# Kernel tuning notes

Hardware: AMD Instinct MI355X
Metric: run time of the kernel (lower is better)

Reference implementation:

```python
import jax, jax.numpy as jnp
import numpy as np

LN_EPS = 1e-5

def _layer_norm(x, g, b):
    mu = jnp.mean(x, axis=-1, keepdims=True)
    var = jnp.mean(jnp.square(x - mu), axis=-1, keepdims=True)
    return (x - mu) * jax.lax.rsqrt(var + LN_EPS) * g + b

def setup_inputs() -> dict:
    key = jax.random.key(0)
    ks = jax.random.split(key, 12)
    B, L, E, H, W = 4, 1024, 1024, 16, 128
    s = 0.02
    return {
        "x": jax.random.normal(ks[0], (B, L, E), dtype=jnp.float32),
        "in_proj_w": jax.random.normal(ks[1], (3 * E, E), dtype=jnp.float32) * s,
        "in_proj_b": jnp.zeros((3 * E,), dtype=jnp.float32),
        "out_proj_w": jax.random.normal(ks[2], (E, E), dtype=jnp.float32) * s,
        "out_proj_b": jnp.zeros((E,), dtype=jnp.float32),
        "ln1_g": jnp.ones((E,), dtype=jnp.float32),
        "ln1_b": jnp.zeros((E,), dtype=jnp.float32),
        "w1": jax.random.normal(ks[3], (4 * E, E), dtype=jnp.float32) * s,
        "b1": jnp.zeros((4 * E,), dtype=jnp.float32),
        "w2": jax.random.normal(ks[4], (E, 4 * E), dtype=jnp.float32) * s,
        "b2": jnp.zeros((E,), dtype=jnp.float32),
        "ln2_g": jnp.ones((E,), dtype=jnp.float32),
        "ln2_b": jnp.zeros((E,), dtype=jnp.float32),
        "n_head": 16,
        "window_size": 128,
    }

def reference(x, in_proj_w, in_proj_b, out_proj_w, out_proj_b,
              ln1_g, ln1_b, w1, b1, w2, b2, ln2_g, ln2_b,
              n_head, window_size):
    B, L, E = x.shape
    H = n_head
    D = E // H
    # qkv projection (torch Linear convention: y = x @ W.T + b)
    qkv = jnp.einsum('ble,fe->blf', x, in_proj_w) + in_proj_b  # [B,L,3E]
    q, k, v = jnp.split(qkv, 3, axis=-1)
    q = q.reshape(B, L, H, D).transpose(0, 2, 1, 3)  # [B,H,L,D]
    k = k.reshape(B, L, H, D).transpose(0, 2, 1, 3)
    v = v.reshape(B, L, H, D).transpose(0, 2, 1, 3)
    scores = jnp.einsum('bhld,bhmd->bhlm', q, k) / np.sqrt(D)  # [B,H,L,L]
    # banded window mask: allowed iff |i-j| <= window_size (same as the double loop)
    idx = jnp.arange(L)
    band = jnp.abs(idx[:, None] - idx[None, :]) <= window_size  # [L,L]
    scores = jnp.where(band[None, None], scores, -jnp.inf)
    attn = jax.nn.softmax(scores, axis=-1)  # [B,H,L,L]
    ctx = jnp.einsum('bhlm,bhmd->bhld', attn, v)  # [B,H,L,D]
    ctx = ctx.transpose(0, 2, 1, 3).reshape(B, L, E)
    attn_out = jnp.einsum('ble,fe->blf', ctx, out_proj_w) + out_proj_b
    attn_weights = jnp.mean(attn, axis=1)  # torch MHA averages heads -> [B,L,L]
    # residual + norm1 (dropout is identity in eval)
    h = _layer_norm(x + attn_out, ln1_g, ln1_b)
    # positionwise FFN
    ff = jnp.einsum('ble,fe->blf', h, w1) + b1
    ff = jax.nn.relu(ff)
    ff = jnp.einsum('blf,ef->ble', ff, w2) + b2
    out = _layer_norm(h + ff, ln2_g, ln2_b)
    return (out, attn_weights)
```

## Files before the change

kernel.cpp:

```cpp
#include <hip/hip_runtime.h>

#define BB 4
#define LL 1024
#define EE 1024
#define HH 16
#define DD 64

typedef __attribute__((ext_vector_type(8))) short short8;
typedef __attribute__((ext_vector_type(4))) float floatx4;

#define PSTR ((size_t)4096 * 1024)

__device__ __forceinline__ float bf2f(short s) {
    union { unsigned u; float f; } c;
    c.u = ((unsigned)(unsigned short)s) << 16;
    return c.f;
}
__device__ __forceinline__ short f2bf(float f) {
    union { float f; unsigned u; } c; c.f = f;
    unsigned r = c.u + 0x7fffu + ((c.u >> 16) & 1u);
    return (short)(r >> 16);
}

__device__ __forceinline__ void async_copy16(const void* g, void* l) {
    __builtin_amdgcn_global_load_lds(
        (const __attribute__((address_space(1))) unsigned int*)g,
        (__attribute__((address_space(3))) unsigned int*)l, 16, 0, 0);
}

__global__ __launch_bounds__(256) void cvt5(
    const float* __restrict__ x, const float* __restrict__ wqkv,
    const float* __restrict__ wo, const float* __restrict__ w1,
    const float* __restrict__ w2,
    short* __restrict__ xb, short* __restrict__ wqkvb, short* __restrict__ wob,
    short* __restrict__ w1b, short* __restrict__ w2b)
{
    int bi = blockIdx.x;
    const float* in; short* out; int base;
    if      (bi <  4096) { in = x;    out = xb;    base = 0;     }
    else if (bi <  7168) { in = wqkv; out = wqkvb; base = 4096;  }
    else if (bi <  8192) { in = wo;   out = wob;   base = 7168;  }
    else if (bi < 12288) { in = w1;   out = w1b;   base = 8192;  }
    else                 { in = w2;   out = w2b;   base = 12288; }
    int i = (bi - base) * 256 + threadIdx.x;
    float4 v = ((const float4*)in)[i];
    unsigned long long u =
          (unsigned long long)(unsigned short)f2bf(v.x)
        | ((unsigned long long)(unsigned short)f2bf(v.y) << 16)
        | ((unsigned long long)(unsigned short)f2bf(v.z) << 32)
        | ((unsigned long long)(unsigned short)f2bf(v.w) << 48);
    ((unsigned long long*)out)[i] = u;
}

template<bool RELU, bool WVT, bool SK>
__global__ __launch_bounds__(512, 2) void gemm256(
    const short* __restrict__ A, const short* __restrict__ Bw,
    const float* __restrict__ bias,
    short* __restrict__ Cb, short* __restrict__ VTp,
    int M, int N, int K, int Ksp)
{
    __shared__ short SH[67584];
    const int tid  = threadIdx.x;
    const int w    = tid >> 6, lane = tid & 63;
    const int fr   = lane & 15, quad = lane >> 4;
    const int wm   = w >> 2,  wn   = w & 3;

    const int gx   = gridDim.x;
    const int flat = blockIdx.y * gx + blockIdx.x;
    const int nwg  = gx * gridDim.y;
    const int q8   = nwg >> 3;
    const int swz  = (flat & 7) * q8 + (flat >> 3);
    const int m0   = (swz % gx) * 256;
    const int n0   = (swz / gx) * 256;

    const int kb = SK ? blockIdx.z * Ksp : 0;
    const int NT = (SK ? Ksp : K) >> 6;

    const int srow = w * 16 + (lane >> 3);
    const int gcol = ((lane & 7) ^ ((lane >> 3) & 7)) * 8;

    auto stage = [&](int s, int h) {
        if (s >= NT) return;
        short* dstb = SH + (s & 1) * 32768 + (h >> 1) * 16384 + (h & 1) * 8192 + w * 1024;
        const short* src = (h < 2)
            ? A  + (size_t)(m0 + h * 128 + srow) * K + kb + s * 64 + gcol
            : Bw + (size_t)(n0 + (h - 2) * 128 + srow) * K + kb + s * 64 + gcol;
        async_copy16(src, dstb);
        async_copy16(src + (size_t)8 * K, dstb + 512);
    };

    floatx4 acc[8][4];
#pragma unroll
    for (int i = 0; i < 8; ++i)
#pragma unroll
        for (int j = 0; j < 4; ++j) acc[i][j] = (floatx4){0.f, 0.f, 0.f, 0.f};

    stage(0, 0); stage(0, 1); stage(0, 2); stage(0, 3);
    stage(1, 0);

    const int posk0 = ((quad    ) ^ (fr & 7)) * 8;
    const int posk1 = ((4 + quad) ^ (fr & 7)) * 8;

    for (int t = 0; t < NT; ++t) {
        if (t < NT - 1) asm volatile("s_waitcnt vmcnt(2)" ::: "memory");
        else            asm volatile("s_waitcnt vmcnt(0)" ::: "memory");
        __builtin_amdgcn_sched_barrier(0);
        __builtin_amdgcn_s_barrier();
        __builtin_amdgcn_sched_barrier(0);

        const short* sA = SH + (t & 1) * 32768 + wm * 8192;
        const short* sB = SH + (t & 1) * 32768 + 16384 + wn * 4096;

        short8 aL[4], aH[4], b0[4], b1[4], a2[4], a3[4];

#pragma unroll
        for (int i = 0; i < 4; ++i) aL[i] = *(const short8*)&sA[(i * 16 + fr) * 64 + posk0];
#pragma unroll
        for (int j = 0; j < 4; ++j) b0[j] = *(const short8*)&sB[(j * 16 + fr) * 64 + posk0];
        stage(t + 1, 1);
        __builtin_amdgcn_s_setprio(1);
#pragma unroll
        for (int i = 0; i < 4; ++i)
#pragma unroll
            for (int j = 0; j < 4; ++j)
                acc[i][j] = __builtin_amdgcn_mfma_f32_16x16x32_bf16(aL[i], b0[j], acc[i][j], 0, 0, 0);
        __builtin_amdgcn_s_setprio(0);

#pragma unroll
        for (int i = 0; i < 4; ++i) aH[i] = *(const short8*)&sA[((i + 4) * 16 + fr) * 64 + posk0];
#pragma unroll
        for (int j = 0; j < 4; ++j) b1[j] = *(const short8*)&sB[(j * 16 + fr) * 64 + posk1];
        stage(t + 1, 2);
        __builtin_amdgcn_s_setprio(1);
#pragma unroll
        for (int i = 0; i < 4; ++i)
#pragma unroll
            for (int j = 0; j < 4; ++j)
                acc[i + 4][j] = __builtin_amdgcn_mfma_f32_16x16x32_bf16(aH[i], b0[j], acc[i + 4][j], 0, 0, 0);
        __builtin_amdgcn_s_setprio(0);

#pragma unroll
        for (int i = 0; i < 4; ++i) a2[i] = *(const short8*)&sA[(i * 16 + fr) * 64 + posk1];
#pragma unroll
        for (int i = 0; i < 4; ++i) a3[i] = *(const short8*)&sA[((i + 4) * 16 + fr) * 64 + posk1];
        stage(t + 1, 3);
        __builtin_amdgcn_s_setprio(1);
#pragma unroll
        for (int i = 0; i < 4; ++i)
#pragma unroll
            for (int j = 0; j < 4; ++j)
                acc[i][j] = __builtin_amdgcn_mfma_f32_16x16x32_bf16(a2[i], b1[j], acc[i][j], 0, 0, 0);
        __builtin_amdgcn_s_setprio(0);

        asm volatile("s_waitcnt lgkmcnt(0)" ::: "memory");
        __builtin_amdgcn_sched_barrier(0);
        __builtin_amdgcn_s_barrier();
        __builtin_amdgcn_sched_barrier(0);

        stage(t + 2, 0);
        __builtin_amdgcn_s_setprio(1);
#pragma unroll
        for (int i = 0; i < 4; ++i)
#pragma unroll
            for (int j = 0; j < 4; ++j)
                acc[i + 4][j] = __builtin_amdgcn_mfma_f32_16x16x32_bf16(a3[i], b1[j], acc[i + 4][j], 0, 0, 0);
        __builtin_amdgcn_s_setprio(0);
    }

    __syncthreads();

    const int cc = lane & 15, rb4 = quad * 4;
#pragma unroll
    for (int i = 0; i < 8; ++i) {
        int row = wm * 128 + i * 16 + rb4;
#pragma unroll
        for (int j = 0; j < 4; ++j) {
            int col = wn * 64 + j * 16 + cc;
            float bv = SK ? 0.0f : bias[n0 + col];
#pragma unroll
            for (int r = 0; r < 4; ++r) {
                float v = acc[i][j][r] + bv;
                if (RELU) v = fmaxf(v, 0.0f);
                SH[(row + r) * 264 + col] = f2bf(v);
            }
        }
    }
    __syncthreads();
    short* Co = Cb + (SK ? (size_t)blockIdx.z * PSTR : 0);
#pragma unroll
    for (int it = 0; it < 16; ++it) {
        int idx = it * 512 + tid;
        int row = idx >> 5, ch = idx & 31;
        short8 v = *(const short8*)&SH[row * 264 + ch * 8];
        *(short8*)&Co[(size_t)(m0 + row) * N + n0 + ch * 8] = v;
        if (WVT) {
            int gc0 = n0 + ch * 8;
            if (gc0 >= 2048) {
                int tok = m0 + row;
                int hc = (gc0 - 2048) >> 6, d0 = (gc0 - 2048) & 63;
                short* vrow = VTp + ((size_t)((tok >> 10) * 16 + hc) * 64 + d0) * 1024 + (tok & 1023);
#pragma unroll
                for (int e = 0; e < 8; ++e) vrow[(size_t)e * 1024] = v[e];
            }
        }
    }
}

template<bool RELU, bool WVT, bool SK>
__global__ __launch_bounds__(256) void gemm_bt(
    const short* __restrict__ A, const short* __restrict__ Bw,
    const float* __restrict__ bias,
    short* __restrict__ Cb, short* __restrict__ VTp,
    int M, int N, int K, int Ksp)
{
    __shared__ union U {
        struct { short As[128 * 64]; short Bs[128 * 64]; } s;
        short Cs[128 * 136];
    } u;
    const int tid  = threadIdx.x;
    const int wave = tid >> 6, lane = tid & 63;
    const int m0 = blockIdx.x * 128, n0 = blockIdx.y * 128;
    const int wm = (wave & 1) * 64, wn = (wave >> 1) * 64;
    const int kbase = SK ? blockIdx.z * Ksp : 0;

    floatx4 acc[4][4];
#pragma unroll
    for (int i = 0; i < 4; ++i)
#pragma unroll
        for (int j = 0; j < 4; ++j) acc[i][j] = (floatx4){0.f, 0.f, 0.f, 0.f};

    const int srow = wave * 8 + (lane >> 3);
    const int scol = (((lane & 7) ^ ((lane >> 3) & 7))) * 8;
    const short* gA = A  + (size_t)(m0 + srow) * K + kbase + scol;
    const short* gB = Bw + (size_t)(n0 + srow) * K + kbase + scol;
    short* lA = u.s.As + wave * 512;
    short* lB = u.s.Bs + wave * 512;

    const int fr = lane & 15, quad = lane >> 4;
    const int kiters = (SK ? Ksp : K) >> 6;
    for (int kt = 0; kt < kiters; ++kt) {
#pragma unroll
        for (int s = 0; s < 4; ++s) {
            async_copy16(gA + (size_t)s * 32 * K, lA + s * 2048);
            async_copy16(gB + (size_t)s * 32 * K, lB + s * 2048);
        }
        gA += 64; gB += 64;
        __syncthreads();
#pragma unroll
        for (int ks = 0; ks < 2; ++ks) {
            short8 af[4], bf[4];
#pragma unroll
            for (int i = 0; i < 4; ++i) {
                int pos = ((ks * 4 + quad) ^ (fr & 7)) * 8;
                af[i] = *(const short8*)&u.s.As[(wm + i * 16 + fr) * 64 + pos];
                bf[i] = *(const short8*)&u.s.Bs[(wn + i * 16 + fr) * 64 + pos];
            }
#pragma unroll
            for (int i = 0; i < 4; ++i)
#pragma unroll
                for (int j = 0; j < 4; ++j)
                    acc[i][j] = __builtin_amdgcn_mfma_f32_16x16x32_bf16(af[i], bf[j], acc[i][j], 0, 0, 0);
        }
        __syncthreads();
    }

    const int cc = lane & 15;
    const int rb = (lane >> 4) * 4;
#pragma unroll
    for (int j = 0; j < 4; ++j) {
        int col = wn + j * 16 + cc;
        float bv = SK ? 0.0f : bias[n0 + col];
#pragma unroll
        for (int i = 0; i < 4; ++i) {
            int row = wm + i * 16 + rb;
#pragma unroll
            for (int r = 0; r < 4; ++r) {
                float v = acc[i][j][r] + bv;
                if (RELU) v = fmaxf(v, 0.0f);
                u.Cs[(row + r) * 136 + col] = f2bf(v);
            }
        }
    }
    __syncthreads();
    short* Co = Cb + (SK ? (size_t)blockIdx.z * PSTR : 0);
    const int trow = tid >> 4, tcol = (tid & 15) * 8;
#pragma unroll
    for (int p = 0; p < 8; ++p) {
        int row = p * 16 + trow;
        short8 vv = *(const short8*)&u.Cs[row * 136 + tcol];
        *(short8*)&Co[(size_t)(m0 + row) * N + n0 + tcol] = vv;
        if (WVT) {
            int gc0 = n0 + tcol;
            if (gc0 >= 2048) {
                int tok = m0 + row;
                int hc = (gc0 - 2048) >> 6, d0 = (gc0 - 2048) & 63;
                short* vrow = VTp + ((size_t)((tok >> 10) * 16 + hc) * 64 + d0) * 1024 + (tok & 1023);
#pragma unroll
                for (int e = 0; e < 8; ++e) vrow[(size_t)e * 1024] = vv[e];
            }
        }
    }
}

__global__ __launch_bounds__(256) void ln_kernel(
    const float* __restrict__ xa, const short* __restrict__ parts, int nparts,
    const float* __restrict__ bias,
    const float* __restrict__ g, const float* __restrict__ beta,
    float* __restrict__ outf, short* __restrict__ outb)
{
    const int row = blockIdx.x;
    const int tid = threadIdx.x;
    float4 va = ((const float4*)(xa + (size_t)row * EE))[tid];
    float4 vb = ((const float4*)bias)[tid];
    float v0 = va.x + vb.x, v1 = va.y + vb.y, v2 = va.z + vb.z, v3 = va.w + vb.w;
#pragma unroll 4
    for (int p = 0; p < nparts; ++p) {
        unsigned long long u8 = ((const unsigned long long*)(parts + p * PSTR + (size_t)row * EE))[tid];
        v0 += bf2f((short)(u8 & 0xffff));
        v1 += bf2f((short)((u8 >> 16) & 0xffff));
        v2 += bf2f((short)((u8 >> 32) & 0xffff));
        v3 += bf2f((short)(u8 >> 48));
    }
    float s  = v0 + v1 + v2 + v3;
    float ss = v0 * v0 + v1 * v1 + v2 * v2 + v3 * v3;
#pragma unroll
    for (int o = 1; o < 64; o <<= 1) { s += __shfl_xor(s, o); ss += __shfl_xor(ss, o); }
    __shared__ float red[8];
    if ((tid & 63) == 0) { red[(tid >> 6) * 2] = s; red[(tid >> 6) * 2 + 1] = ss; }
    __syncthreads();
    s  = red[0] + red[2] + red[4] + red[6];
    ss = red[1] + red[3] + red[5] + red[7];
    float mean = s * (1.0f / EE);
    float var  = ss * (1.0f / EE) - mean * mean;
    float rstd = rsqrtf(var + 1e-5f);
    float4 vg = ((const float4*)g)[tid];
    float4 vt = ((const float4*)beta)[tid];
    float o0 = (v0 - mean) * rstd * vg.x + vt.x;
    float o1 = (v1 - mean) * rstd * vg.y + vt.y;
    float o2 = (v2 - mean) * rstd * vg.z + vt.z;
    float o3 = (v3 - mean) * rstd * vg.w + vt.w;
    if (outf) ((float4*)(outf + (size_t)row * EE))[tid] = make_float4(o0, o1, o2, o3);
    if (outb) {
        unsigned long long u =
              (unsigned long long)(unsigned short)f2bf(o0)
            | ((unsigned long long)(unsigned short)f2bf(o1) << 16)
            | ((unsigned long long)(unsigned short)f2bf(o2) << 32)
            | ((unsigned long long)(unsigned short)f2bf(o3) << 48);
        ((unsigned long long*)(outb + (size_t)row * EE))[tid] = u;
    }
}

__global__ __launch_bounds__(512, 8) void attn_mfma(
    const short* __restrict__ qkv,
    const short* __restrict__ vt,
    short* __restrict__ ctxp,
    short* __restrict__ pb)
{
    __shared__ short Pl[32 * 320];
    __shared__ float Red[4][2][32];
    const int tid = threadIdx.x, wave = tid >> 6, lane = tid & 63;
    const int quad = lane >> 4, mcol = lane & 15;
    const int id = blockIdx.x;
    const int i0 = (id >> 6) * 32, h = id & 15, b = (id >> 4) & 3;
    const int jb0 = i0 - 128;

    const short* qb = qkv + (size_t)(b * 1024) * 3072 + h * 64;
    const short* kb = qb + 1024;

    const int mt = wave >> 2, qtr = wave & 3;
    const short* qrow = qb + (size_t)(i0 + mt * 16 + mcol) * 3072 + quad * 8;
    short8 aq0 = *(const short8*)qrow;
    short8 aq1 = *(const short8*)(qrow + 32);

    floatx4 sacc[5];
#pragma unroll
    for (int c = 0; c < 5; ++c) sacc[c] = (floatx4){0.f, 0.f, 0.f, 0.f};
#pragma unroll
    for (int c = 0; c < 5; ++c) {
        int j = jb0 + (qtr * 5 + c) * 16 + mcol;
        j = min(max(j, 0), 1023);
        const short* kr = kb + (size_t)j * 3072 + quad * 8;
        short8 b0 = *(const short8*)kr;
        short8 b1 = *(const short8*)(kr + 32);
        sacc[c] = __builtin_amdgcn_mfma_f32_16x16x32_bf16(aq0, b0, sacc[c], 0, 0, 0);
        sacc[c] = __builtin_amdgcn_mfma_f32_16x16x32_bf16(aq1, b1, sacc[c], 0, 0, 0);
    }

    const int row0 = mt * 16 + quad * 4;
#pragma unroll
    for (int r = 0; r < 4; ++r) {
        int row = row0 + r;
        float m = -1e30f;
#pragma unroll
        for (int c = 0; c < 5; ++c) {
            int jo = (qtr * 5 + c) * 16 + mcol;
            bool val = (jo >= row) && (jo <= row + 256) && ((unsigned)(jb0 + jo) < 1024u);
            float s = val ? sacc[c][r] * 0.125f : -1e30f;
            sacc[c][r] = s;
            m = fmaxf(m, s);
        }
        m = fmaxf(m, __shfl_xor(m, 1));
        m = fmaxf(m, __shfl_xor(m, 2));
        m = fmaxf(m, __shfl_xor(m, 4));
        m = fmaxf(m, __shfl_xor(m, 8));
        if (mcol == 0) Red[qtr][0][row] = m;
    }
    __syncthreads();
#pragma unroll
    for (int r = 0; r < 4; ++r) {
        int row = row0 + r;
        float M = fmaxf(fmaxf(Red[0][0][row], Red[1][0][row]),
                        fmaxf(Red[2][0][row], Red[3][0][row]));
        float l = 0.f;
#pragma unroll
        for (int c = 0; c < 5; ++c) {
            float p = __expf(sacc[c][r] - M);
            sacc[c][r] = p;
            l += p;
        }
        l += __shfl_xor(l, 1);
        l += __shfl_xor(l, 2);
        l += __shfl_xor(l, 4);
        l += __shfl_xor(l, 8);
        if (mcol == 0) Red[qtr][1][row] = l;
    }
    __syncthreads();
#pragma unroll
    for (int r = 0; r < 4; ++r) {
        int row = row0 + r;
        float inv = 1.0f / (Red[0][1][row] + Red[1][1][row] +
                            Red[2][1][row] + Red[3][1][row]);
#pragma unroll
        for (int c = 0; c < 5; ++c) {
            int jo = (qtr * 5 + c) * 16 + mcol;
            Pl[row * 320 + (((jo >> 3) ^ (row & 7)) * 8) + (jo & 7)] = f2bf(sacc[c][r] * inv);
        }
    }
    __syncthreads();

    const int pmt = wave & 1, dt = wave >> 1;
    floatx4 cacc = (floatx4){0.f, 0.f, 0.f, 0.f};
    const short* vrow = vt + ((size_t)((b * 16 + h) * 64) + dt * 16 + mcol) * 1024;
    const int prow = (pmt * 16 + mcol) * 320;
#pragma unroll
    for (int jc = 0; jc < 10; ++jc) {
        short8 ap = *(const short8*)&Pl[prow + (((jc * 4 + quad) ^ (mcol & 7)) * 8)];
        int jg = jb0 + jc * 32 + quad * 8;
        if ((unsigned)jg >= 1024u) jg = 0;
        short8 bv = *(const short8*)(vrow + jg);
        cacc = __builtin_amdgcn_mfma_f32_16x16x32_bf16(ap, bv, cacc, 0, 0, 0);
    }

    short* pbb = pb + ((size_t)((b * 16 + h) * 1024) + i0) * 320;
    for (int t = tid; t < 1280; t += 512) {
        int row = t / 40, c = t - row * 40;
        short8 v = *(const short8*)&Pl[row * 320 + ((c ^ (row & 7)) * 8)];
        *(short8*)&pbb[(size_t)t * 8] = v;
    }
    __syncthreads();

    short* Ct = Pl;
    const int colc = dt * 16 + mcol;
#pragma unroll
    for (int r = 0; r < 4; ++r)
        Ct[(pmt * 16 + quad * 4 + r) * 72 + colc] = f2bf(cacc[r]);
    __syncthreads();
    short* cb = ctxp + (size_t)(b * 1024 + i0) * 1024 + h * 64;
    for (int t = tid; t < 256; t += 512) {
        int row = t >> 3, c = t & 7;
        short8 v = *(const short8*)&Ct[row * 72 + c * 8];
        *(short8*)&cb[(size_t)row * 1024 + c * 8] = v;
    }
}

__global__ __launch_bounds__(256) void pb_reduce(const short* __restrict__ pb,
                                                 float* __restrict__ aw)
{
    const int i = blockIdx.x & 1023, b = blockIdx.x >> 10;
    const int i0 = i & ~31;
    __shared__ short P[16 * 320];
    for (int t = threadIdx.x; t < 640; t += 256) {
        int hh = t / 40, c = t - hh * 40;
        ((short8*)P)[t] = *(const short8*)(pb +
            ((size_t)((b * 16 + hh) * 1024) + i) * 320 + c * 8);
    }
    __syncthreads();
    float* row = aw + ((size_t)(b * 1024) + i) * 1024;
    for (int j = threadIdx.x; j < 1024; j += 256) {
        int jo = j - i0 + 128;
        float s = 0.f;
        if ((unsigned)jo < 320u) {
#pragma unroll
            for (int hh = 0; hh < 16; ++hh)
                s += bf2f(P[hh * 320 + jo]);
            s *= (1.0f / 16.0f);
        }
        row[j] = s;
    }
}

extern "C" void kernel_launch(void* const* d_in, const int* in_sizes, int n_in,
                              void* d_out, int out_size, void* d_ws, size_t ws_size,
                              hipStream_t stream) {
    const float* x    = (const float*)d_in[0];
    const float* wqkv = (const float*)d_in[1];
    const float* bqkv = (const float*)d_in[2];
    const float* wo   = (const float*)d_in[3];
    const float* bo   = (const float*)d_in[4];
    const float* g1   = (const float*)d_in[5];
    const float* be1  = (const float*)d_in[6];
    const float* w1   = (const float*)d_in[7];
    const float* bb1  = (const float*)d_in[8];
    const float* w2   = (const float*)d_in[9];
    const float* bb2  = (const float*)d_in[10];
    const float* g2   = (const float*)d_in[11];
    const float* be2  = (const float*)d_in[12];

    char* ws = (char*)d_ws;
    size_t off = 0;
    auto take = [&](size_t bytes) {
        void* p = ws + off;
        off += (bytes + 255) & ~(size_t)255;
        return p;
    };
    short* xb     = (short*)take((size_t)4096 * 1024 * 2);
    short* wqkv_b = (short*)take((size_t)3072 * 1024 * 2);
    short* wo_b   = (short*)take((size_t)1024 * 1024 * 2);
    short* w1_b   = (short*)take((size_t)4096 * 1024 * 2);
    short* w2_b   = (short*)take((size_t)1024 * 4096 * 2);
    short* qkv_b  = (short*)take((size_t)4096 * 3072 * 2);
    short* ctx_b  = (short*)take((size_t)4096 * 1024 * 2);
    short* ff2_p  = qkv_b;
    short* attn_p = (short*)take((size_t)2 * 4096 * 1024 * 2);
    float* h_f    = (float*)take((size_t)4096 * 1024 * 4);
    short* vt_ws  = (short*)h_f;
    short* h_b    = (short*)take((size_t)4096 * 1024 * 2);
    short* pb_ws  = (short*)take((size_t)4 * 16 * 1024 * 320 * 2);
    short* ff_b   = pb_ws;

    float* out_f = (float*)d_out;
    float* attnW = (float*)d_out + (size_t)4 * 1024 * 1024;

    cvt5<<<16384, 256, 0, stream>>>(x, wqkv, wo, w1, w2, xb, wqkv_b, wo_b, w1_b, w2_b);

    gemm256<false, true, false><<<dim3(16, 12), 512, 0, stream>>>(
        xb, wqkv_b, bqkv, qkv_b, vt_ws, 4096, 3072, 1024, 1024);

    attn_mfma<<<2048, 512, 0, stream>>>(qkv_b, vt_ws, ctx_b, pb_ws);

    pb_reduce<<<4096, 256, 0, stream>>>(pb_ws, attnW);

    gemm_bt<false, false, true><<<dim3(32, 8, 2), 256, 0, stream>>>(
        ctx_b, wo_b, nullptr, attn_p, nullptr, 4096, 1024, 1024, 512);

    ln_kernel<<<4096, 256, 0, stream>>>(x, attn_p, 2, bo, g1, be1, h_f, h_b);

    gemm256<true, false, false><<<dim3(16, 16), 512, 0, stream>>>(
        h_b, w1_b, bb1, ff_b, nullptr, 4096, 4096, 1024, 1024);

    gemm256<false, false, true><<<dim3(16, 4, 4), 512, 0, stream>>>(
        ff_b, w2_b, nullptr, ff2_p, nullptr, 4096, 1024, 4096, 1024);

    ln_kernel<<<4096, 256, 0, stream>>>(h_f, ff2_p, 4, bb2, g2, be2, out_f, nullptr);
}
```

Baseline: 349.7 us.

## Restructure gemm256 pipeline with per-phase barriers and move V transpose to separate kernel

After: 342.6 us. -2.0%, faster.

```diff
diff --git a/kernel.cpp b/kernel.cpp
--- a/kernel.cpp
+++ b/kernel.cpp
@@ -52,11 +52,11 @@
     ((unsigned long long*)out)[i] = u;
 }
 
-template<bool RELU, bool WVT, bool SK>
+template<bool RELU, bool SK>
 __global__ __launch_bounds__(512, 2) void gemm256(
     const short* __restrict__ A, const short* __restrict__ Bw,
     const float* __restrict__ bias,
-    short* __restrict__ Cb, short* __restrict__ VTp,
+    short* __restrict__ Cb,
     int M, int N, int K, int Ksp)
 {
     __shared__ short SH[67584];
@@ -96,18 +96,13 @@
         for (int j = 0; j < 4; ++j) acc[i][j] = (floatx4){0.f, 0.f, 0.f, 0.f};
 
     stage(0, 0); stage(0, 1); stage(0, 2); stage(0, 3);
-    stage(1, 0);
+    asm volatile("s_waitcnt vmcnt(0)" ::: "memory");
+    __builtin_amdgcn_s_barrier();
 
     const int posk0 = ((quad    ) ^ (fr & 7)) * 8;
     const int posk1 = ((4 + quad) ^ (fr & 7)) * 8;
 
     for (int t = 0; t < NT; ++t) {
-        if (t < NT - 1) asm volatile("s_waitcnt vmcnt(2)" ::: "memory");
-        else            asm volatile("s_waitcnt vmcnt(0)" ::: "memory");
-        __builtin_amdgcn_sched_barrier(0);
-        __builtin_amdgcn_s_barrier();
-        __builtin_amdgcn_sched_barrier(0);
-
         const short* sA = SH + (t & 1) * 32768 + wm * 8192;
         const short* sB = SH + (t & 1) * 32768 + 16384 + wn * 4096;
 
@@ -117,7 +112,10 @@
         for (int i = 0; i < 4; ++i) aL[i] = *(const short8*)&sA[(i * 16 + fr) * 64 + posk0];
 #pragma unroll
         for (int j = 0; j < 4; ++j) b0[j] = *(const short8*)&sB[(j * 16 + fr) * 64 + posk0];
-        stage(t + 1, 1);
+        stage(t + 1, 0); stage(t + 1, 1);
+        __builtin_amdgcn_s_barrier();
+        asm volatile("s_waitcnt lgkmcnt(0)" ::: "memory");
+        __builtin_amdgcn_sched_barrier(0);
         __builtin_amdgcn_s_setprio(1);
 #pragma unroll
         for (int i = 0; i < 4; ++i)
@@ -125,12 +123,15 @@
             for (int j = 0; j < 4; ++j)
                 acc[i][j] = __builtin_amdgcn_mfma_f32_16x16x32_bf16(aL[i], b0[j], acc[i][j], 0, 0, 0);
         __builtin_amdgcn_s_setprio(0);
+        __builtin_amdgcn_sched_barrier(0);
+        __builtin_amdgcn_s_barrier();
 
 #pragma unroll
         for (int i = 0; i < 4; ++i) aH[i] = *(const short8*)&sA[((i + 4) * 16 + fr) * 64 + posk0];
-#pragma unroll
-        for (int j = 0; j < 4; ++j) b1[j] = *(const short8*)&sB[(j * 16 + fr) * 64 + posk1];
-        stage(t + 1, 2);
+        stage(t + 1, 2); stage(t + 1, 3);
+        __builtin_amdgcn_s_barrier();
+        asm volatile("s_waitcnt lgkmcnt(0)" ::: "memory");
+        __builtin_amdgcn_sched_barrier(0);
         __builtin_amdgcn_s_setprio(1);
 #pragma unroll
         for (int i = 0; i < 4; ++i)
@@ -138,12 +139,16 @@
             for (int j = 0; j < 4; ++j)
                 acc[i + 4][j] = __builtin_amdgcn_mfma_f32_16x16x32_bf16(aH[i], b0[j], acc[i + 4][j], 0, 0, 0);
         __builtin_amdgcn_s_setprio(0);
+        __builtin_amdgcn_sched_barrier(0);
+        __builtin_amdgcn_s_barrier();
 
 #pragma unroll
         for (int i = 0; i < 4; ++i) a2[i] = *(const short8*)&sA[(i * 16 + fr) * 64 + posk1];
 #pragma unroll
-        for (int i = 0; i < 4; ++i) a3[i] = *(const short8*)&sA[((i + 4) * 16 + fr) * 64 + posk1];
-        stage(t + 1, 3);
+        for (int j = 0; j < 4; ++j) b1[j] = *(const short8*)&sB[(j * 16 + fr) * 64 + posk1];
+        __builtin_amdgcn_s_barrier();
+        asm volatile("s_waitcnt lgkmcnt(0)" ::: "memory");
+        __builtin_amdgcn_sched_barrier(0);
         __builtin_amdgcn_s_setprio(1);
 #pragma unroll
         for (int i = 0; i < 4; ++i)
@@ -151,13 +156,15 @@
             for (int j = 0; j < 4; ++j)
                 acc[i][j] = __builtin_amdgcn_mfma_f32_16x16x32_bf16(a2[i], b1[j], acc[i][j], 0, 0, 0);
         __builtin_amdgcn_s_setprio(0);
-
+        __builtin_amdgcn_sched_barrier(0);
+        __builtin_amdgcn_s_barrier();
+
+#pragma unroll
+        for (int i = 0; i < 4; ++i) a3[i] = *(const short8*)&sA[((i + 4) * 16 + fr) * 64 + posk1];
+        asm volatile("s_waitcnt vmcnt(0)" ::: "memory");
+        __builtin_amdgcn_s_barrier();
         asm volatile("s_waitcnt lgkmcnt(0)" ::: "memory");
         __builtin_amdgcn_sched_barrier(0);
-        __builtin_amdgcn_s_barrier();
-        __builtin_amdgcn_sched_barrier(0);
-
-        stage(t + 2, 0);
         __builtin_amdgcn_s_setprio(1);
 #pragma unroll
         for (int i = 0; i < 4; ++i)
@@ -165,6 +172,8 @@
             for (int j = 0; j < 4; ++j)
                 acc[i + 4][j] = __builtin_amdgcn_mfma_f32_16x16x32_bf16(a3[i], b1[j], acc[i + 4][j], 0, 0, 0);
         __builtin_amdgcn_s_setprio(0);
+        __builtin_amdgcn_sched_barrier(0);
+        __builtin_amdgcn_s_barrier();
     }
 
     __syncthreads();
@@ -193,24 +202,40 @@
         int row = idx >> 5, ch = idx & 31;
         short8 v = *(const short8*)&SH[row * 264 + ch * 8];
         *(short8*)&Co[(size_t)(m0 + row) * N + n0 + ch * 8] = v;
-        if (WVT) {
-            int gc0 = n0 + ch * 8;
-            if (gc0 >= 2048) {
-                int tok = m0 + row;
-                int hc = (gc0 - 2048) >> 6, d0 = (gc0 - 2048) & 63;
-                short* vrow = VTp + ((size_t)((tok >> 10) * 16 + hc) * 64 + d0) * 1024 + (tok & 1023);
-#pragma unroll
-                for (int e = 0; e < 8; ++e) vrow[(size_t)e * 1024] = v[e];
-            }
-        }
-    }
-}
-
-template<bool RELU, bool WVT, bool SK>
+    }
+}
+
+__global__ __launch_bounds__(256) void vtrans(const short* __restrict__ qkv,
+                                              short* __restrict__ vt)
+{
+    int id = blockIdx.x;
+    int tb = id & 15, h = (id >> 4) & 15, b = id >> 8;
+    __shared__ short T[64 * 72];
+    const short* src = qkv + (size_t)(b * 1024 + tb * 64) * 3072 + 2048 + h * 64;
+    int tok = threadIdx.x >> 2;
+    int c8  = threadIdx.x & 3;
+#pragma unroll
+    for (int q = 0; q < 2; ++q) {
+        int d0 = (c8 * 2 + q) * 8;
+        short8 v = *(const short8*)&src[(size_t)tok * 3072 + d0];
+#pragma unroll
+        for (int e = 0; e < 8; ++e) T[(d0 + e) * 72 + tok] = v[e];
+    }
+    __syncthreads();
+    short* dst = vt + (size_t)((b * 16 + h) * 64) * 1024 + tb * 64;
+    int d = threadIdx.x >> 2, cq = threadIdx.x & 3;
+#pragma unroll
+    for (int q = 0; q < 2; ++q) {
+        int t0 = (cq * 2 + q) * 8;
+        *(short8*)&dst[(size_t)d * 1024 + t0] = *(const short8*)&T[d * 72 + t0];
+    }
+}
+
+template<bool RELU, bool SK>
 __global__ __launch_bounds__(256) void gemm_bt(
     const short* __restrict__ A, const short* __restrict__ Bw,
     const float* __restrict__ bias,
-    short* __restrict__ Cb, short* __restrict__ VTp,
+    short* __restrict__ Cb,
     int M, int N, int K, int Ksp)
 {
     __shared__ union U {
@@ -289,16 +314,6 @@
         int row = p * 16 + trow;
         short8 vv = *(const short8*)&u.Cs[row * 136 + tcol];
         *(short8*)&Co[(size_t)(m0 + row) * N + n0 + tcol] = vv;
-        if (WVT) {
-            int gc0 = n0 + tcol;
-            if (gc0 >= 2048) {
-                int tok = m0 + row;
-                int hc = (gc0 - 2048) >> 6, d0 = (gc0 - 2048) & 63;
-                short* vrow = VTp + ((size_t)((tok >> 10) * 16 + hc) * 64 + d0) * 1024 + (tok & 1023);
-#pragma unroll
-                for (int e = 0; e < 8; ++e) vrow[(size_t)e * 1024] = vv[e];
-            }
-        }
     }
 }
 
@@ -543,23 +558,25 @@
 
     cvt5<<<16384, 256, 0, stream>>>(x, wqkv, wo, w1, w2, xb, wqkv_b, wo_b, w1_b, w2_b);
 
-    gemm256<false, true, false><<<dim3(16, 12), 512, 0, stream>>>(
-        xb, wqkv_b, bqkv, qkv_b, vt_ws, 4096, 3072, 1024, 1024);
+    gemm256<false, false><<<dim3(16, 12), 512, 0, stream>>>(
+        xb, wqkv_b, bqkv, qkv_b, 4096, 3072, 1024, 1024);
+
+    vtrans<<<1024, 256, 0, stream>>>(qkv_b, vt_ws);
 
     attn_mfma<<<2048, 512, 0, stream>>>(qkv_b, vt_ws, ctx_b, pb_ws);
 
     pb_reduce<<<4096, 256, 0, stream>>>(pb_ws, attnW);
 
-    gemm_bt<false, false, true><<<dim3(32, 8, 2), 256, 0, stream>>>(
-        ctx_b, wo_b, nullptr, attn_p, nullptr, 4096, 1024, 1024, 512);
+    gemm_bt<false, true><<<dim3(32, 8, 2), 256, 0, stream>>>(
+        ctx_b, wo_b, nullptr, attn_p, 4096, 1024, 1024, 512);
 
     ln_kernel<<<4096, 256, 0, stream>>>(x, attn_p, 2, bo, g1, be1, h_f, h_b);
 
-    gemm256<true, false, false><<<dim3(16, 16), 512, 0, stream>>>(
-        h_b, w1_b, bb1, ff_b, nullptr, 4096, 4096, 1024, 1024);
-
-    gemm256<false, false, true><<<dim3(16, 4, 4), 512, 0, stream>>>(
-        ff_b, w2_b, nullptr, ff2_p, nullptr, 4096, 1024, 4096, 1024);
+    gemm256<true, false><<<dim3(16, 16), 512, 0, stream>>>(
+        h_b, w1_b, bb1, ff_b, 4096, 4096, 1024, 1024);
+
+    gemm256<false, true><<<dim3(16, 4, 4), 512, 0, stream>>>(
+        ff_b, w2_b, nullptr, ff2_p, 4096, 1024, 4096, 1024);
 
     ln_kernel<<<4096, 256, 0, stream>>>(h_f, ff2_p, 4, bb2, g2, be2, out_f, nullptr);
 }
```
